# Kernel tuning notes

Measured on AMD Instinct MI355X. Metric: run time of the kernel, lower is better.

The kernel has to match this reference:

```python
import jax, jax.numpy as jnp
import numpy as np

B = 1024      # num graphs
NPG = 128     # nodes per graph
N = B * NPG
EPG = 512     # edges per graph
E = B * EPG
D = 64
MAX_STEPS = 4
S = MAX_STEPS + 1   # max_steps + stop-step offset
T = 1.0
TB = 1.0
NEG = -1e30
STOP = -1


def setup_inputs() -> dict:
    key = jax.random.key(0)
    ks = jax.random.split(key, 24)
    edge_batch = jnp.repeat(jnp.arange(B, dtype=jnp.int32), EPG)
    src = jax.random.randint(ks[0], (E,), 0, NPG, dtype=jnp.int32) + edge_batch * NPG
    dst = jax.random.randint(ks[1], (E,), 0, NPG, dtype=jnp.int32) + edge_batch * NPG
    edge_index = jnp.stack([src, dst])
    sc = 1.0 / np.sqrt(D)
    p = lambda k, shape: (jax.random.normal(k, shape, jnp.float32) * sc)
    return dict(
        node_tokens=p(ks[2], (N, D)), edge_emb=p(ks[3], (E, D)),
        Wf1=p(ks[4], (D, D)), Wnf=p(ks[5], (D, D)), Wf2=p(ks[6], (D, D)),
        bf=jnp.zeros((D,), jnp.float32), wf=p(ks[7], (D,)),
        Wb1=p(ks[8], (D, D)), Wnb=p(ks[9], (D, D)), Wb2=p(ks[10], (D, D)),
        bb=jnp.zeros((D,), jnp.float32), wb=p(ks[11], (D,)),
        w_stop=p(ks[12], (D,)), b_stop=jnp.zeros((), jnp.float32),
        Ws=p(ks[13], (D, D)), Wu=p(ks[14], (D, D)), bu=jnp.zeros((D,), jnp.float32),
        edge_index=edge_index, edge_batch=edge_batch,
    )


def reference(node_tokens, edge_emb, Wf1, Wnf, Wf2, bf, wf,
              Wb1, Wnb, Wb2, bb, wb, w_stop, b_stop, Ws, Wu, bu,
              edge_index, edge_batch):
    esrc, edst = edge_index[0], edge_index[1]
    # state-independent part of the edge scores (precomputed once; faithful math)
    base_f = edge_emb @ Wf1 + node_tokens[esrc] @ Wnf + bf   # [E,D]
    base_b = edge_emb @ Wb1 + node_tokens[edst] @ Wnb + bb   # [E,D]
    g_ids = jnp.arange(B, dtype=jnp.int32)
    eidx = jnp.arange(E, dtype=jnp.int32)

    def seg_lse(x, valid):
        # per-graph logsumexp over valid edges (grad-safe masking)
        xm = jnp.where(valid, x, NEG)
        m = jax.ops.segment_max(xm, edge_batch, num_segments=B)
        xc = jnp.where(valid, x - m[edge_batch], 0.0)
        s = jax.ops.segment_sum(jnp.where(valid, jnp.exp(xc), 0.0), edge_batch, num_segments=B)
        return m + jnp.log(jnp.maximum(s, 1e-30))

    def step_fn(carry, k):
        state_vec, active, used, done, steps, stopn = carry
        valid = (esrc == active[edge_batch]) & (~used) & (~done[edge_batch])
        allow_stop = (~done) & (steps < MAX_STEPS)
        # forward edge scores + stop logit
        h = jax.nn.relu(base_f + (state_vec @ Wf2)[edge_batch])   # [E,D]
        score = h @ wf                                            # [E]
        stop_logit = state_vec @ w_stop + b_stop                  # [B]
        x = score / T
        lse_e = seg_lse(x, valid)
        stop_t = jnp.where(allow_stop, stop_logit / T, NEG)
        Z = jnp.logaddexp(lse_e, stop_t)
        logp_edge = x - Z[edge_batch]
        logp_stop = jnp.where(allow_stop, stop_logit / T - Z, 0.0)
        has_edge = jax.ops.segment_sum(valid.astype(jnp.int32), edge_batch, num_segments=B) > 0
        # gumbel-max sampling with scatter_max semantics
        ke, ksn = jax.random.split(k)
        se = jnp.where(valid, logp_edge + jax.random.gumbel(ke, (E,)), NEG)
        ss = jnp.where(allow_stop, logp_stop + jax.random.gumbel(ksn, (B,)), NEG)
        m = jax.ops.segment_max(se, edge_batch, num_segments=B)
        amax = jax.ops.segment_min(jnp.where(se == m[edge_batch], eidx, E), edge_batch, num_segments=B)
        amax = jnp.where(has_edge, amax, 0).astype(jnp.int32)
        m = jnp.where(has_edge, m, NEG)
        choose_stop = (ss > m) | (~has_edge)
        actions = jnp.where(choose_stop | done, STOP, amax)
        log_pf = jnp.where(choose_stop, logp_stop, logp_edge[amax])
        log_pf = jnp.where(done, 0.0, log_pf)
        take_edge = (actions >= 0) & (~done)
        stopping = choose_stop & (~done)
        stopn = jnp.where((stopn < 0) & stopping, active - g_ids * NPG, stopn)
        # state encoder update (masked)
        rel = edge_emb[amax]                                      # [B,D]
        new_state = jnp.tanh(state_vec @ Ws + rel @ Wu + bu)
        state_vec = jnp.where(take_edge[:, None], new_state, state_vec)
        # env step
        new_active = jnp.where(take_edge, edst[amax], active)
        used = used.at[amax].max(take_edge)
        steps = steps + take_edge.astype(jnp.int32)
        new_done = done | stopping
        # backward policy log-prob over edges incoming to the new active node
        bvalid = edst == new_active[edge_batch]
        hb = jax.nn.relu(base_b + (state_vec @ Wb2)[edge_batch])
        xb = (hb @ wb) / TB
        lse_b = seg_lse(xb, bvalid)
        log_pb = jnp.where(take_edge, xb[amax] - lse_b, 0.0)
        return (state_vec, new_active, used, new_done, steps, stopn), (actions, log_pf, log_pb)

    init = (
        jnp.zeros((B, D), jnp.float32),      # state_vec
        g_ids * NPG,                          # active node (global) = graph start node
        jnp.zeros((E,), bool),                # used_edge_mask
        jnp.zeros((B,), bool),                # done
        jnp.zeros((B,), jnp.int32),           # step_counts
        jnp.full((B,), STOP, jnp.int32),      # stop_node_locals
    )
    keys = jax.random.split(jax.random.key(42), S)
    (state_vec, active, used, done, steps, stopn), ys = jax.lax.scan(step_fn, init, keys)
    actions_seq = ys[0].T      # [B,S]
    log_pf_steps = ys[1].T     # [B,S]
    log_pb_steps = ys[2].T     # [B,S]
    stopn = jnp.where(stopn < 0, active - g_ids * NPG, stopn)   # backfill stop nodes
    return (actions_seq, log_pf_steps.sum(1), log_pf_steps, log_pb_steps,
            used, stopn, steps.astype(jnp.float32))
```

## Files before the change

### kernel.cpp

```cpp
#include <hip/hip_runtime.h>
#include <hip/hip_bf16.h>
#include <cstdint>

#define NBLK 1024
#define NPG  128
#define EPG  512
#define DD   64
#define NSTEP 5
#define ETOT (NBLK*EPG)
#define NEGF (-1e30f)
#define WAVES 4
#define MAXDEG 32

#define OA  0
#define OLS 5120
#define OPF 6144
#define OPB 11264
#define OU  16384
#define OSN 540672
#define OST 541696

struct KeysArg {
  uint32_t ke0[NSTEP], ke1[NSTEP];
  uint32_t ks0[NSTEP], ks1[NSTEP];
};

__host__ __device__ inline uint32_t rotl32(uint32_t x, int r){ return (x<<r)|(x>>(32-r)); }

__host__ __device__ inline void tf2x32(uint32_t k0, uint32_t k1, uint32_t& x0, uint32_t& x1){
  uint32_t k2 = k0 ^ k1 ^ 0x1BD11BDAu;
  x0 += k0; x1 += k1;
  x0+=x1; x1=rotl32(x1,13); x1^=x0;
  x0+=x1; x1=rotl32(x1,15); x1^=x0;
  x0+=x1; x1=rotl32(x1,26); x1^=x0;
  x0+=x1; x1=rotl32(x1, 6); x1^=x0;
  x0+=k1; x1+=k2+1u;
  x0+=x1; x1=rotl32(x1,17); x1^=x0;
  x0+=x1; x1=rotl32(x1,29); x1^=x0;
  x0+=x1; x1=rotl32(x1,16); x1^=x0;
  x0+=x1; x1=rotl32(x1,24); x1^=x0;
  x0+=k2; x1+=k0+2u;
  x0+=x1; x1=rotl32(x1,13); x1^=x0;
  x0+=x1; x1=rotl32(x1,15); x1^=x0;
  x0+=x1; x1=rotl32(x1,26); x1^=x0;
  x0+=x1; x1=rotl32(x1, 6); x1^=x0;
  x0+=k0; x1+=k1+3u;
  x0+=x1; x1=rotl32(x1,17); x1^=x0;
  x0+=x1; x1=rotl32(x1,29); x1^=x0;
  x0+=x1; x1=rotl32(x1,16); x1^=x0;
  x0+=x1; x1=rotl32(x1,24); x1^=x0;
  x0+=k1; x1+=k2+4u;
  x0+=x1; x1=rotl32(x1,13); x1^=x0;
  x0+=x1; x1=rotl32(x1,15); x1^=x0;
  x0+=x1; x1=rotl32(x1,26); x1^=x0;
  x0+=x1; x1=rotl32(x1, 6); x1^=x0;
  x0+=k2; x1+=k0+5u;
}

__device__ inline float gumbel_from_bits(uint32_t bits){
  float f = __uint_as_float((bits>>9) | 0x3f800000u) - 1.0f;
  const float tiny = 1.17549435e-38f;
  float u = fmaxf(tiny, f * (1.0f - tiny) + tiny);
  return -logf(-logf(u));
}

__device__ inline float gumbel_part(uint32_t k0, uint32_t k1, uint32_t idx){
  uint32_t x0 = 0u, x1 = idx;
  tf2x32(k0, k1, x0, x1);
  return gumbel_from_bits(x0 ^ x1);
}

__device__ inline float wsum(float x){
  #pragma unroll
  for (int off = 32; off; off >>= 1) x += __shfl_xor(x, off, 64);
  return x;
}

__device__ __forceinline__ void wsum4(float& x0, float& x1, float& x2, float& x3){
  #pragma unroll
  for (int off = 32; off; off >>= 1){
    x0 += __shfl_xor(x0, off, 64);
    x1 += __shfl_xor(x1, off, 64);
    x2 += __shfl_xor(x2, off, 64);
    x3 += __shfl_xor(x3, off, 64);
  }
}

__device__ __forceinline__ float rdlane(float v, int i){
  return __int_as_float(__builtin_amdgcn_readlane(__float_as_int(v), i));
}
__device__ __forceinline__ int rdlane_i(int v, int i){
  return __builtin_amdgcn_readlane(v, i);
}

__device__ __forceinline__ float matvec_col(const float* __restrict__ W, float v, int lane){
  float a0=0.f, a1=0.f, a2=0.f, a3=0.f;
  #pragma unroll 8
  for (int i = 0; i < DD; i += 4){
    a0 = fmaf(rdlane(v, i  ), W[(i  )*DD+lane], a0);
    a1 = fmaf(rdlane(v, i+1), W[(i+1)*DD+lane], a1);
    a2 = fmaf(rdlane(v, i+2), W[(i+2)*DD+lane], a2);
    a3 = fmaf(rdlane(v, i+3), W[(i+3)*DD+lane], a3);
  }
  return (a0+a1)+(a2+a3);
}

__device__ __forceinline__ void matvec4(const float* __restrict__ W,
                                        float v0, float v1, float v2, float v3,
                                        int lane, float o[4]){
  float acc[4][4] = {{0,0,0,0},{0,0,0,0},{0,0,0,0},{0,0,0,0}};
  #pragma unroll 8
  for (int i = 0; i < DD; i += 4){
    #pragma unroll
    for (int t = 0; t < 4; t++){
      float w  = W[(i+t)*DD+lane];
      acc[0][t] = fmaf(rdlane(v0, i+t), w, acc[0][t]);
      acc[1][t] = fmaf(rdlane(v1, i+t), w, acc[1][t]);
      acc[2][t] = fmaf(rdlane(v2, i+t), w, acc[2][t]);
      acc[3][t] = fmaf(rdlane(v3, i+t), w, acc[3][t]);
    }
  }
  #pragma unroll
  for (int c = 0; c < 4; c++)
    o[c] = (acc[c][0]+acc[c][1])+(acc[c][2]+acc[c][3]);
}

__global__ void __launch_bounds__(256, 4)
gfn_fused(const float* __restrict__ node_tokens,
          const float* __restrict__ edge_emb,
          const float* __restrict__ Wf1, const float* __restrict__ Wnf, const float* __restrict__ Wf2,
          const float* __restrict__ bf,  const float* __restrict__ wf,
          const float* __restrict__ Wb1, const float* __restrict__ Wnb, const float* __restrict__ Wb2,
          const float* __restrict__ bb,  const float* __restrict__ wb,
          const float* __restrict__ w_stop, const float* __restrict__ b_stop,
          const float* __restrict__ Ws,  const float* __restrict__ Wu, const float* __restrict__ bu,
          const int* __restrict__ e_src, const int* __restrict__ e_dst,
          float* __restrict__ out, KeysArg keys)
{
  const int g    = blockIdx.x;
  const int tid  = threadIdx.x;
  const int lane = tid & 63;
  const int wave = tid >> 6;
  const int ebase = g * EPG;

  __shared__ uint8_t  srcL[EPG], dstL[EPG];
  __shared__ uint16_t listO[EPG], listI[EPG];
  __shared__ int cntO[NPG], cntI[NPG], begO[NPG], begI[NPG];
  __shared__ uint8_t usedL[EPG];
  __shared__ float st_sh[DD];
  __shared__ float u_sh[DD], nt_sh[DD], acs_sh[DD];
  __shared__ float ntb_sh[DD], ntN_sh[DD], uN_sh[DD], ubB_sh[DD];
  __shared__ float xcF[MAXDEG], gmF[MAXDEG], xcB[MAXDEG];
  __shared__ float sl_sh, xbb_sh;

  for (int j = tid; j < EPG; j += 256){
    srcL[j] = (uint8_t)(e_src[ebase+j] - g*NPG);
    dstL[j] = (uint8_t)(e_dst[ebase+j] - g*NPG);
    usedL[j] = 0;
  }
  for (int n = tid; n < NPG; n += 256){ cntO[n]=0; cntI[n]=0; }
  if (tid < DD) st_sh[tid] = 0.f;
  __syncthreads();

  for (int j = tid; j < EPG; j += 256){
    atomicAdd(&cntO[srcL[j]], 1);
    atomicAdd(&cntI[dstL[j]], 1);
  }
  __syncthreads();

  if (wave == 0){
    int n0 = lane*2, n1 = n0+1;
    int c0O=cntO[n0], c1O=cntO[n1], sO=c0O+c1O;
    int c0I=cntI[n0], c1I=cntI[n1], sI=c0I+c1I;
    int xO=sO, xI=sI;
    #pragma unroll
    for (int off=1; off<64; off<<=1){
      int tO=__shfl_up(xO,off,64), tI=__shfl_up(xI,off,64);
      if (lane>=off){ xO+=tO; xI+=tI; }
    }
    begO[n0]=xO-sO; begO[n1]=xO-c1O;
    begI[n0]=xI-sI; begI[n1]=xI-c1I;
  }
  __syncthreads();
  for (int n = tid; n < NPG; n += 256){ cntO[n]=0; cntI[n]=0; }
  __syncthreads();

  for (int ph = 0; ph < WAVES; ph++){
    if (wave == ph){
      #pragma unroll
      for (int h = 0; h < 2; h++){
        int j = ph*128 + h*64 + lane;
        int sL = srcL[j]; int p = atomicAdd(&cntO[sL],1); listO[begO[sL]+p] = (uint16_t)j;
        int dL = dstL[j]; int q = atomicAdd(&cntI[dL],1); listI[begI[dL]+q] = (uint16_t)j;
      }
    }
    __syncthreads();
  }

  const float bf_l = bf[lane], wf_l = wf[lane];
  const float bb_l = bb[lane], wb_l = wb[lane];
  const float bu_l = bu[lane], wst_l = w_stop[lane];
  const float bstop = b_stop[0];

  float gsv;
  {
    uint32_t k0 = keys.ks0[0], k1 = keys.ks1[0];
    #pragma unroll
    for (int s5 = 1; s5 < NSTEP; s5++)
      if (lane == s5){ k0 = keys.ks0[s5]; k1 = keys.ks1[s5]; }
    gsv = (lane < NSTEP) ? gumbel_part(k0, k1, (uint32_t)g) : 0.f;
  }

  bool done = false;
  int stepsC = 0, stopn = -1, activeL = 0;
  float lpf_sum = 0.f;
  int bOF = begO[0], dOF = min(cntO[0], MAXDEG);

  {
    float st_v = st_sh[lane];
    if (wave == 0)      u_sh[lane]   = matvec_col(Wf2, st_v, lane);
    else if (wave == 1){ float ntv = node_tokens[(size_t)(g*NPG+0)*DD+lane];
                         nt_sh[lane] = matvec_col(Wnf, ntv, lane); }
    else if (wave == 2) acs_sh[lane] = matvec_col(Ws, st_v, lane);
    else {
      float sl = wsum(st_v * wst_l) + bstop;
      if (lane == 0) sl_sh = sl;
      if (lane < dOF)
        gmF[lane] = gumbel_part(keys.ke0[0], keys.ke1[0], (uint32_t)(ebase + listO[bOF+lane]));
    }
    __syncthreads();
    if (wave >= 2){
      for (int c = wave-2; c < (dOF+3)>>2; c += 2){
        int el[4]; float v[4];
        #pragma unroll
        for (int t = 0; t < 4; t++){
          int k = c*4 + t;
          el[t] = listO[bOF + min(k, dOF-1)];
          v[t]  = edge_emb[(size_t)(ebase+el[t])*DD + lane];
        }
        float o[4], x[4];
        matvec4(Wf1, v[0], v[1], v[2], v[3], lane, o);
        #pragma unroll
        for (int t = 0; t < 4; t++) x[t] = fmaxf(o[t] + nt_sh[lane] + bf_l + u_sh[lane], 0.f) * wf_l;
        wsum4(x[0], x[1], x[2], x[3]);
        #pragma unroll
        for (int t = 0; t < 4; t++){
          int k = c*4 + t;
          if (k < dOF && lane == 0) xcF[k] = usedL[el[t]] ? NEGF : x[t];
        }
      }
    }
    __syncthreads();
  }

  for (int s = 0; s < NSTEP; s++){
    float act_out = -1.f, lpf_out = 0.f, lpb_out = 0.f;
    if (!done){
      float xr = (lane < MAXDEG) ? xcF[lane] : NEGF;
      float gr = (lane < MAXDEG) ? gmF[lane] : 0.f;
      int   er = (lane < dOF)    ? (int)listO[bOF + lane] : -1;
      float sl = sl_sh;

      float m1 = NEGF; int nvalid = 0;
      for (int k=0;k<dOF;k++){ float xk=rdlane(xr,k); if (xk!=NEGF){ m1=fmaxf(m1,xk); nvalid++; } }
      float ex = expf(xr - m1);
      float ssum = 0.f;
      for (int k=0;k<dOF;k++){ float xk=rdlane(xr,k); if (xk!=NEGF) ssum += rdlane(ex,k); }
      const bool has_edge = nvalid > 0;
      float lse_e = m1 + logf(fmaxf(ssum, 1e-30f));
      const bool allow_stop = (stepsC < 4);
      float stop_t = allow_stop ? sl : NEGF;
      float amx = fmaxf(lse_e, stop_t);
      float Z = amx + log1pf(expf(-fabsf(lse_e - stop_t)));

      float mbest = NEGF; int elbest = -1; float xbest = 0.f;
      for (int k=0;k<dOF;k++){
        float xk = rdlane(xr,k);
        if (xk == NEGF) continue;
        float se = (xk - Z) + rdlane(gr,k);
        if (se > mbest){ mbest = se; elbest = rdlane_i(er,k); xbest = xk; }
      }
      float gs = rdlane(gsv, s);
      float ss = allow_stop ? (sl - Z) + gs : NEGF;
      float mcmp = has_edge ? mbest : NEGF;
      const bool choose_stop = (ss > mcmp) || (!has_edge);
      float logp_stop = allow_stop ? (sl - Z) : 0.f;
      const bool take_edge = !choose_stop;

      act_out = choose_stop ? -1.f : (float)(ebase + elbest);
      lpf_out = choose_stop ? logp_stop : (xbest - Z);
      if (choose_stop && stopn < 0) stopn = activeL;

      if (take_edge){
        const int newA = dstL[elbest];
        const bool more = (s < NSTEP-1);
        const int bI  = begI[newA], dIc = min(cntI[newA], MAXDEG);
        const int bON = begO[newA];
        const int dON = more ? min(cntO[newA], MAXDEG) : 0;

        float vPre[4]; int elPre[4]; bool pre = false; int c0;
        if (wave == 2 || wave == 0){
          c0 = (wave==2 ? 0 : 1);
          if (c0 < ((dIc+3)>>2)){
            pre = true;
            #pragma unroll
            for (int t = 0; t < 4; t++){
              int k = c0*4 + t;
              elPre[t] = listI[bI + min(k, dIc-1)];
              vPre[t]  = edge_emb[(size_t)(ebase+elPre[t])*DD + lane];
            }
          }
        } else {
          c0 = (wave==3 ? 0 : 1);
          if (c0 < ((dON+3)>>2)){
            pre = true;
            #pragma unroll
            for (int t = 0; t < 4; t++){
              int k = c0*4 + t;
              elPre[t] = listO[bON + min(k, dON-1)];
              vPre[t]  = edge_emb[(size_t)(ebase+elPre[t])*DD + lane];
            }
          }
        }

        if (wave == 0){
          float rv = edge_emb[(size_t)(ebase+elbest)*DD + lane];
          float acr = matvec_col(Wu, rv, lane);
          st_sh[lane] = tanhf(acs_sh[lane] + acr + bu_l);
          if (lane == 0) usedL[elbest] = 1;
        } else if (wave == 1){
          float nbv = node_tokens[(size_t)(g*NPG + newA)*DD + lane];
          ntb_sh[lane] = matvec_col(Wnb, nbv, lane);
        } else if (wave == 2){
          if (more){
            float nbv = node_tokens[(size_t)(g*NPG + newA)*DD + lane];
            ntN_sh[lane] = matvec_col(Wnf, nbv, lane);
          }
        }
        activeL = newA; stepsC++;
        __syncthreads();

        float stp = st_sh[lane];
        if (wave == 0){
          if (more) uN_sh[lane] = matvec_col(Wf2, stp, lane);
        } else if (wave == 1){
          ubB_sh[lane] = matvec_col(Wb2, stp, lane);
        } else if (wave == 2){
          if (more) acs_sh[lane] = matvec_col(Ws, stp, lane);
        } else {
          if (more){
            float s2 = wsum(stp * wst_l) + bstop;
            if (lane == 0) sl_sh = s2;
            if (lane < dON)
              gmF[lane] = gumbel_part(keys.ke0[s+1], keys.ke1[s+1],
                                      (uint32_t)(ebase + listO[bON+lane]));
          }
        }
        __syncthreads();

        if (wave == 2 || wave == 0){
          for (int c = c0; c < (dIc+3)>>2; c += 2){
            int el[4]; float v[4];
            if (pre && c == c0){
              #pragma unroll
              for (int t = 0; t < 4; t++){ el[t] = elPre[t]; v[t] = vPre[t]; }
            } else {
              #pragma unroll
              for (int t = 0; t < 4; t++){
                int k = c*4 + t;
                el[t] = listI[bI + min(k, dIc-1)];
                v[t]  = edge_emb[(size_t)(ebase+el[t])*DD + lane];
              }
            }
            float o[4], xb[4];
            matvec4(Wb1, v[0], v[1], v[2], v[3], lane, o);
            #pragma unroll
            for (int t = 0; t < 4; t++) xb[t] = fmaxf(o[t] + ntb_sh[lane] + bb_l + ubB_sh[lane], 0.f) * wb_l;
            wsum4(xb[0], xb[1], xb[2], xb[3]);
            #pragma unroll
            for (int t = 0; t < 4; t++){
              int k = c*4 + t;
              if (k < dIc && lane == 0){
                xcB[k] = xb[t];
                if (el[t] == elbest) xbb_sh = xb[t];
              }
            }
          }
        } else {
          for (int c = c0; c < (dON+3)>>2; c += 2){
            int el[4]; float v[4];
            if (pre && c == c0){
              #pragma unroll
              for (int t = 0; t < 4; t++){ el[t] = elPre[t]; v[t] = vPre[t]; }
            } else {
              #pragma unroll
              for (int t = 0; t < 4; t++){
                int k = c*4 + t;
                el[t] = listO[bON + min(k, dON-1)];
                v[t]  = edge_emb[(size_t)(ebase+el[t])*DD + lane];
              }
            }
            float o[4], x[4];
            matvec4(Wf1, v[0], v[1], v[2], v[3], lane, o);
            #pragma unroll
            for (int t = 0; t < 4; t++) x[t] = fmaxf(o[t] + ntN_sh[lane] + bf_l + uN_sh[lane], 0.f) * wf_l;
            wsum4(x[0], x[1], x[2], x[3]);
            #pragma unroll
            for (int t = 0; t < 4; t++){
              int k = c*4 + t;
              if (k < dON && lane == 0) xcF[k] = usedL[el[t]] ? NEGF : x[t];
            }
          }
        }
        __syncthreads();

        float xbr = (lane < MAXDEG) ? xcB[lane] : 0.f;
        float m2 = NEGF;
        for (int k=0;k<dIc;k++) m2 = fmaxf(m2, rdlane(xbr,k));
        float ex2 = expf(xbr - m2);
        float s2 = 0.f;
        for (int k=0;k<dIc;k++) s2 += rdlane(ex2,k);
        float lse_b = m2 + logf(fmaxf(s2, 1e-30f));
        lpb_out = xbb_sh - lse_b;

        bOF = bON; dOF = dON;
      }
      done = done || choose_stop;
    }

    if (tid == 0){
      out[OA  + g*NSTEP + s] = act_out;
      out[OPF + g*NSTEP + s] = lpf_out;
      out[OPB + g*NSTEP + s] = lpb_out;
    }
    lpf_sum += lpf_out;
  }

  if (tid == 0){
    out[OLS + g] = lpf_sum;
    int sn = (stopn < 0) ? activeL : stopn;
    out[OSN + g] = (float)sn;
    out[OST + g] = (float)stepsC;
  }
  for (int j = tid; j < EPG; j += 256)
    out[OU + ebase + j] = usedL[j] ? 1.0f : 0.0f;
}

extern "C" void kernel_launch(void* const* d_in, const int* in_sizes, int n_in,
                              void* d_out, int out_size, void* d_ws, size_t ws_size,
                              hipStream_t stream)
{
  (void)in_sizes; (void)n_in; (void)out_size; (void)d_ws; (void)ws_size;

  KeysArg K;
  for (uint32_t s = 0; s < NSTEP; s++){
    uint32_t a = 0u, b = s;
    tf2x32(0u, 42u, a, b);
    uint32_t e0 = 0u, e1 = 0u;
    tf2x32(a, b, e0, e1);
    uint32_t s0 = 0u, s1 = 1u;
    tf2x32(a, b, s0, s1);
    K.ke0[s] = e0; K.ke1[s] = e1;
    K.ks0[s] = s0; K.ks1[s] = s1;
  }

  const int* eidx = (const int*)d_in[17];
  gfn_fused<<<dim3(NBLK), dim3(256), 0, stream>>>(
      (const float*)d_in[0],  (const float*)d_in[1],
      (const float*)d_in[2],  (const float*)d_in[3],  (const float*)d_in[4],
      (const float*)d_in[5],  (const float*)d_in[6],
      (const float*)d_in[7],  (const float*)d_in[8],  (const float*)d_in[9],
      (const float*)d_in[10], (const float*)d_in[11],
      (const float*)d_in[12], (const float*)d_in[13],
      (const float*)d_in[14], (const float*)d_in[15], (const float*)d_in[16],
      eidx, eidx + ETOT,
      (float*)d_out, K);
}
```

Measured before the change: 78.35 us.

## Replicate per-step state matvecs in every wave and cut barriers to one per step

Each wave now computes the state update, stop logit, gumbel noise and its own node/state projections redundantly in registers, so the shared-memory staging buffers go away. The score buffers are double-buffered by step parity, which lets each step run with a single __syncthreads instead of three. The forward masking now also excludes the just-chosen edge locally, because usedL may not be visible yet. The cost is more redundant matvec work per wave, which raises ALU load and register pressure in exchange for fewer barrier stalls.

```diff
diff --git a/kernel.cpp b/kernel.cpp
--- a/kernel.cpp
+++ b/kernel.cpp
@@ -142,16 +142,15 @@
   const int lane = tid & 63;
   const int wave = tid >> 6;
   const int ebase = g * EPG;
+  const bool isBwd = (wave == 0) || (wave == 2);
 
   __shared__ uint8_t  srcL[EPG], dstL[EPG];
   __shared__ uint16_t listO[EPG], listI[EPG];
   __shared__ int cntO[NPG], cntI[NPG], begO[NPG], begI[NPG];
   __shared__ uint8_t usedL[EPG];
-  __shared__ float st_sh[DD];
-  __shared__ float u_sh[DD], nt_sh[DD], acs_sh[DD];
-  __shared__ float ntb_sh[DD], ntN_sh[DD], uN_sh[DD], ubB_sh[DD];
-  __shared__ float xcF[MAXDEG], gmF[MAXDEG], xcB[MAXDEG];
-  __shared__ float sl_sh, xbb_sh;
+  __shared__ float xcF[2][MAXDEG];
+  __shared__ float xcB[2][MAXDEG];
+  __shared__ float xbb_sh[2];
 
   for (int j = tid; j < EPG; j += 256){
     srcL[j] = (uint8_t)(e_src[ebase+j] - g*NPG);
@@ -159,7 +158,6 @@
     usedL[j] = 0;
   }
   for (int n = tid; n < NPG; n += 256){ cntO[n]=0; cntI[n]=0; }
-  if (tid < DD) st_sh[tid] = 0.f;
   __syncthreads();
 
   for (int j = tid; j < EPG; j += 256){
@@ -216,21 +214,20 @@
   float lpf_sum = 0.f;
   int bOF = begO[0], dOF = min(cntO[0], MAXDEG);
 
+  float st_v = 0.f;
+  float acs_reg, sl_reg, gm_reg;
+
   {
-    float st_v = st_sh[lane];
-    if (wave == 0)      u_sh[lane]   = matvec_col(Wf2, st_v, lane);
-    else if (wave == 1){ float ntv = node_tokens[(size_t)(g*NPG+0)*DD+lane];
-                         nt_sh[lane] = matvec_col(Wnf, ntv, lane); }
-    else if (wave == 2) acs_sh[lane] = matvec_col(Ws, st_v, lane);
-    else {
-      float sl = wsum(st_v * wst_l) + bstop;
-      if (lane == 0) sl_sh = sl;
-      if (lane < dOF)
-        gmF[lane] = gumbel_part(keys.ke0[0], keys.ke1[0], (uint32_t)(ebase + listO[bOF+lane]));
-    }
-    __syncthreads();
-    if (wave >= 2){
-      for (int c = wave-2; c < (dOF+3)>>2; c += 2){
+    float u0  = matvec_col(Wf2, st_v, lane);
+    float ntv = node_tokens[(size_t)(g*NPG + 0)*DD + lane];
+    float nt0 = matvec_col(Wnf, ntv, lane);
+    acs_reg = matvec_col(Ws, st_v, lane);
+    sl_reg  = wsum(st_v * wst_l) + bstop;
+    gm_reg  = (lane < dOF)
+            ? gumbel_part(keys.ke0[0], keys.ke1[0], (uint32_t)(ebase + listO[bOF+lane]))
+            : 0.f;
+    if (!isBwd){
+      for (int c = (wave==3 ? 0 : 1); c < (dOF+3)>>2; c += 2){
         int el[4]; float v[4];
         #pragma unroll
         for (int t = 0; t < 4; t++){
@@ -241,12 +238,12 @@
         float o[4], x[4];
         matvec4(Wf1, v[0], v[1], v[2], v[3], lane, o);
         #pragma unroll
-        for (int t = 0; t < 4; t++) x[t] = fmaxf(o[t] + nt_sh[lane] + bf_l + u_sh[lane], 0.f) * wf_l;
+        for (int t = 0; t < 4; t++) x[t] = fmaxf(o[t] + nt0 + bf_l + u0, 0.f) * wf_l;
         wsum4(x[0], x[1], x[2], x[3]);
         #pragma unroll
         for (int t = 0; t < 4; t++){
           int k = c*4 + t;
-          if (k < dOF && lane == 0) xcF[k] = usedL[el[t]] ? NEGF : x[t];
+          if (k < dOF && lane == 0) xcF[0][k] = usedL[el[t]] ? NEGF : x[t];
         }
       }
     }
@@ -254,12 +251,15 @@
   }
 
   for (int s = 0; s < NSTEP; s++){
+    const int par = s & 1;
     float act_out = -1.f, lpf_out = 0.f, lpb_out = 0.f;
+    bool take_edge = false, stopped_now = false;
+    int dIc = 0;
+
     if (!done){
-      float xr = (lane < MAXDEG) ? xcF[lane] : NEGF;
-      float gr = (lane < MAXDEG) ? gmF[lane] : 0.f;
+      float xr = (lane < MAXDEG) ? xcF[par][lane] : NEGF;
       int   er = (lane < dOF)    ? (int)listO[bOF + lane] : -1;
-      float sl = sl_sh;
+      float sl = sl_reg;
 
       float m1 = NEGF; int nvalid = 0;
       for (int k=0;k<dOF;k++){ float xk=rdlane(xr,k); if (xk!=NEGF){ m1=fmaxf(m1,xk); nvalid++; } }
@@ -277,7 +277,7 @@
       for (int k=0;k<dOF;k++){
         float xk = rdlane(xr,k);
         if (xk == NEGF) continue;
-        float se = (xk - Z) + rdlane(gr,k);
+        float se = (xk - Z) + rdlane(gm_reg,k);
         if (se > mbest){ mbest = se; elbest = rdlane_i(er,k); xbest = xk; }
       }
       float gs = rdlane(gsv, s);
@@ -285,7 +285,8 @@
       float mcmp = has_edge ? mbest : NEGF;
       const bool choose_stop = (ss > mcmp) || (!has_edge);
       float logp_stop = allow_stop ? (sl - Z) : 0.f;
-      const bool take_edge = !choose_stop;
+      take_edge = !choose_stop;
+      stopped_now = choose_stop;
 
       act_out = choose_stop ? -1.f : (float)(ebase + elbest);
       lpf_out = choose_stop ? logp_stop : (xbest - Z);
@@ -294,13 +295,15 @@
       if (take_edge){
         const int newA = dstL[elbest];
         const bool more = (s < NSTEP-1);
-        const int bI  = begI[newA], dIc = min(cntI[newA], MAXDEG);
+        const int bI  = begI[newA]; dIc = min(cntI[newA], MAXDEG);
         const int bON = begO[newA];
         const int dON = more ? min(cntO[newA], MAXDEG) : 0;
 
-        float vPre[4]; int elPre[4]; bool pre = false; int c0;
-        if (wave == 2 || wave == 0){
-          c0 = (wave==2 ? 0 : 1);
+        float rv  = edge_emb[(size_t)(ebase+elbest)*DD + lane];
+        float nbv = node_tokens[(size_t)(g*NPG + newA)*DD + lane];
+        float vPre[4]; int elPre[4]; bool pre = false; int c0 = 0;
+        if (isBwd){
+          c0 = (wave==0 ? 0 : 1);
           if (c0 < ((dIc+3)>>2)){
             pre = true;
             #pragma unroll
@@ -310,7 +313,7 @@
               vPre[t]  = edge_emb[(size_t)(ebase+elPre[t])*DD + lane];
             }
           }
-        } else {
+        } else if (more){
           c0 = (wave==3 ? 0 : 1);
           if (c0 < ((dON+3)>>2)){
             pre = true;
@@ -323,42 +326,28 @@
           }
         }
 
-        if (wave == 0){
-          float rv = edge_emb[(size_t)(ebase+elbest)*DD + lane];
-          float acr = matvec_col(Wu, rv, lane);
-          st_sh[lane] = tanhf(acs_sh[lane] + acr + bu_l);
-          if (lane == 0) usedL[elbest] = 1;
-        } else if (wave == 1){
-          float nbv = node_tokens[(size_t)(g*NPG + newA)*DD + lane];
-          ntb_sh[lane] = matvec_col(Wnb, nbv, lane);
-        } else if (wave == 2){
-          if (more){
-            float nbv = node_tokens[(size_t)(g*NPG + newA)*DD + lane];
-            ntN_sh[lane] = matvec_col(Wnf, nbv, lane);
-          }
-        }
+        float acr = matvec_col(Wu, rv, lane);
+        st_v = tanhf(acs_reg + acr + bu_l);
+        float d1 = 0.f, d2 = 0.f;
+        if (isBwd){
+          d1 = matvec_col(Wnb, nbv, lane);
+          d2 = matvec_col(Wb2, st_v, lane);
+        } else if (more){
+          d1 = matvec_col(Wnf, nbv, lane);
+          d2 = matvec_col(Wf2, st_v, lane);
+        }
+        if (more){
+          acs_reg = matvec_col(Ws, st_v, lane);
+          sl_reg  = wsum(st_v * wst_l) + bstop;
+          gm_reg  = (lane < dON)
+                  ? gumbel_part(keys.ke0[s+1], keys.ke1[s+1],
+                                (uint32_t)(ebase + listO[bON+lane]))
+                  : 0.f;
+        }
+        if (tid == 0) usedL[elbest] = 1;
         activeL = newA; stepsC++;
-        __syncthreads();
-
-        float stp = st_sh[lane];
-        if (wave == 0){
-          if (more) uN_sh[lane] = matvec_col(Wf2, stp, lane);
-        } else if (wave == 1){
-          ubB_sh[lane] = matvec_col(Wb2, stp, lane);
-        } else if (wave == 2){
-          if (more) acs_sh[lane] = matvec_col(Ws, stp, lane);
-        } else {
-          if (more){
-            float s2 = wsum(stp * wst_l) + bstop;
-            if (lane == 0) sl_sh = s2;
-            if (lane < dON)
-              gmF[lane] = gumbel_part(keys.ke0[s+1], keys.ke1[s+1],
-                                      (uint32_t)(ebase + listO[bON+lane]));
-          }
-        }
-        __syncthreads();
-
-        if (wave == 2 || wave == 0){
+
+        if (isBwd){
           for (int c = c0; c < (dIc+3)>>2; c += 2){
             int el[4]; float v[4];
             if (pre && c == c0){
@@ -375,18 +364,18 @@
             float o[4], xb[4];
             matvec4(Wb1, v[0], v[1], v[2], v[3], lane, o);
             #pragma unroll
-            for (int t = 0; t < 4; t++) xb[t] = fmaxf(o[t] + ntb_sh[lane] + bb_l + ubB_sh[lane], 0.f) * wb_l;
+            for (int t = 0; t < 4; t++) xb[t] = fmaxf(o[t] + d1 + bb_l + d2, 0.f) * wb_l;
             wsum4(xb[0], xb[1], xb[2], xb[3]);
             #pragma unroll
             for (int t = 0; t < 4; t++){
               int k = c*4 + t;
               if (k < dIc && lane == 0){
-                xcB[k] = xb[t];
-                if (el[t] == elbest) xbb_sh = xb[t];
+                xcB[par][k] = xb[t];
+                if (el[t] == elbest) xbb_sh[par] = xb[t];
               }
             }
           }
-        } else {
+        } else if (more){
           for (int c = c0; c < (dON+3)>>2; c += 2){
             int el[4]; float v[4];
             if (pre && c == c0){
@@ -403,30 +392,33 @@
             float o[4], x[4];
             matvec4(Wf1, v[0], v[1], v[2], v[3], lane, o);
             #pragma unroll
-            for (int t = 0; t < 4; t++) x[t] = fmaxf(o[t] + ntN_sh[lane] + bf_l + uN_sh[lane], 0.f) * wf_l;
+            for (int t = 0; t < 4; t++) x[t] = fmaxf(o[t] + d1 + bf_l + d2, 0.f) * wf_l;
             wsum4(x[0], x[1], x[2], x[3]);
             #pragma unroll
             for (int t = 0; t < 4; t++){
               int k = c*4 + t;
-              if (k < dON && lane == 0) xcF[k] = usedL[el[t]] ? NEGF : x[t];
+              if (k < dON && lane == 0)
+                xcF[par^1][k] = (usedL[el[t]] || el[t] == elbest) ? NEGF : x[t];
             }
           }
         }
-        __syncthreads();
-
-        float xbr = (lane < MAXDEG) ? xcB[lane] : 0.f;
-        float m2 = NEGF;
-        for (int k=0;k<dIc;k++) m2 = fmaxf(m2, rdlane(xbr,k));
-        float ex2 = expf(xbr - m2);
-        float s2 = 0.f;
-        for (int k=0;k<dIc;k++) s2 += rdlane(ex2,k);
-        float lse_b = m2 + logf(fmaxf(s2, 1e-30f));
-        lpb_out = xbb_sh - lse_b;
-
         bOF = bON; dOF = dON;
       }
-      done = done || choose_stop;
-    }
+    }
+
+    __syncthreads();
+
+    if (!done && take_edge){
+      float xbr = (lane < MAXDEG) ? xcB[par][lane] : 0.f;
+      float m2 = NEGF;
+      for (int k=0;k<dIc;k++) m2 = fmaxf(m2, rdlane(xbr,k));
+      float ex2 = expf(xbr - m2);
+      float s2 = 0.f;
+      for (int k=0;k<dIc;k++) s2 += rdlane(ex2,k);
+      float lse_b = m2 + logf(fmaxf(s2, 1e-30f));
+      lpb_out = xbb_sh[par] - lse_b;
+    }
+    done = done || stopped_now;
 
     if (tid == 0){
       out[OA  + g*NSTEP + s] = act_out;
```

Measured after the change: 96.08 us. 1.23x slower.

## Widen block to 8 waves and speculatively precompute per-candidate-edge matvecs

Applied to the files above, without the earlier changes.

Doubles the block to 512 threads and dedicates extra waves to precompute, for every candidate outgoing edge, the Wu, Wnb and Wnf matvecs of the edge embedding and destination node token, stored in shared memory. Once the edge is chosen, the state update and node projections become lookups rather than serial matvecs on the critical path. Part of the backward and forward edge-score matvecs is also started before the barrier to overlap with the state matvecs. In exchange it does extra speculative work for edges that are never chosen, uses more shared memory and registers, and launches with a 512-thread occupancy hint of 6 blocks.

```diff
diff --git a/kernel.cpp b/kernel.cpp
--- a/kernel.cpp
+++ b/kernel.cpp
@@ -9,8 +9,8 @@
 #define NSTEP 5
 #define ETOT (NBLK*EPG)
 #define NEGF (-1e30f)
-#define WAVES 4
 #define MAXDEG 32
+#define TPB 512
 
 #define OA  0
 #define OLS 5120
@@ -125,7 +125,7 @@
     o[c] = (acc[c][0]+acc[c][1])+(acc[c][2]+acc[c][3]);
 }
 
-__global__ void __launch_bounds__(256, 4)
+__global__ void __launch_bounds__(512, 6)
 gfn_fused(const float* __restrict__ node_tokens,
           const float* __restrict__ edge_emb,
           const float* __restrict__ Wf1, const float* __restrict__ Wnf, const float* __restrict__ Wf2,
@@ -147,22 +147,22 @@
   __shared__ uint16_t listO[EPG], listI[EPG];
   __shared__ int cntO[NPG], cntI[NPG], begO[NPG], begI[NPG];
   __shared__ uint8_t usedL[EPG];
-  __shared__ float st_sh[DD];
-  __shared__ float u_sh[DD], nt_sh[DD], acs_sh[DD];
-  __shared__ float ntb_sh[DD], ntN_sh[DD], uN_sh[DD], ubB_sh[DD];
+  __shared__ float uN_sh[DD], ubB_sh[DD], acs_sh[DD], ntN_sh[DD];
+  __shared__ float wuv[MAXDEG][DD];
+  __shared__ float wnbv[MAXDEG][DD];
+  __shared__ float wnfv[MAXDEG][DD];
   __shared__ float xcF[MAXDEG], gmF[MAXDEG], xcB[MAXDEG];
   __shared__ float sl_sh, xbb_sh;
 
-  for (int j = tid; j < EPG; j += 256){
+  for (int j = tid; j < EPG; j += TPB){
     srcL[j] = (uint8_t)(e_src[ebase+j] - g*NPG);
     dstL[j] = (uint8_t)(e_dst[ebase+j] - g*NPG);
     usedL[j] = 0;
   }
-  for (int n = tid; n < NPG; n += 256){ cntO[n]=0; cntI[n]=0; }
-  if (tid < DD) st_sh[tid] = 0.f;
+  for (int n = tid; n < NPG; n += TPB){ cntO[n]=0; cntI[n]=0; }
   __syncthreads();
 
-  for (int j = tid; j < EPG; j += 256){
+  for (int j = tid; j < EPG; j += TPB){
     atomicAdd(&cntO[srcL[j]], 1);
     atomicAdd(&cntI[dstL[j]], 1);
   }
@@ -182,17 +182,14 @@
     begI[n0]=xI-sI; begI[n1]=xI-c1I;
   }
   __syncthreads();
-  for (int n = tid; n < NPG; n += 256){ cntO[n]=0; cntI[n]=0; }
+  for (int n = tid; n < NPG; n += TPB){ cntO[n]=0; cntI[n]=0; }
   __syncthreads();
 
-  for (int ph = 0; ph < WAVES; ph++){
+  for (int ph = 0; ph < 8; ph++){
     if (wave == ph){
-      #pragma unroll
-      for (int h = 0; h < 2; h++){
-        int j = ph*128 + h*64 + lane;
-        int sL = srcL[j]; int p = atomicAdd(&cntO[sL],1); listO[begO[sL]+p] = (uint16_t)j;
-        int dL = dstL[j]; int q = atomicAdd(&cntI[dL],1); listI[begI[dL]+q] = (uint16_t)j;
-      }
+      int j = ph*64 + lane;
+      int sL = srcL[j]; int p = atomicAdd(&cntO[sL],1); listO[begO[sL]+p] = (uint16_t)j;
+      int dL = dstL[j]; int q = atomicAdd(&cntI[dL],1); listI[begI[dL]+q] = (uint16_t)j;
     }
     __syncthreads();
   }
@@ -217,37 +214,69 @@
   int bOF = begO[0], dOF = min(cntO[0], MAXDEG);
 
   {
-    float st_v = st_sh[lane];
-    if (wave == 0)      u_sh[lane]   = matvec_col(Wf2, st_v, lane);
-    else if (wave == 1){ float ntv = node_tokens[(size_t)(g*NPG+0)*DD+lane];
-                         nt_sh[lane] = matvec_col(Wnf, ntv, lane); }
-    else if (wave == 2) acs_sh[lane] = matvec_col(Ws, st_v, lane);
-    else {
-      float sl = wsum(st_v * wst_l) + bstop;
+    if (wave == 0)      uN_sh[lane] = matvec_col(Wf2, 0.f, lane);
+    else if (wave == 1){ float ntv = node_tokens[(size_t)(g*NPG)*DD + lane];
+                         ntN_sh[lane] = matvec_col(Wnf, ntv, lane); }
+    else if (wave == 2) acs_sh[lane] = matvec_col(Ws, 0.f, lane);
+    else if (wave == 3){
+      float sl = wsum(0.f * wst_l) + bstop;
       if (lane == 0) sl_sh = sl;
       if (lane < dOF)
         gmF[lane] = gumbel_part(keys.ke0[0], keys.ke1[0], (uint32_t)(ebase + listO[bOF+lane]));
     }
     __syncthreads();
-    if (wave >= 2){
-      for (int c = wave-2; c < (dOF+3)>>2; c += 2){
+    const int nfc = (dOF+3)>>2;
+    if (wave == 4){
+      for (int c = 0; c < nfc; c++){
         int el[4]; float v[4];
         #pragma unroll
         for (int t = 0; t < 4; t++){
-          int k = c*4 + t;
-          el[t] = listO[bOF + min(k, dOF-1)];
+          el[t] = listO[bOF + min(c*4+t, dOF-1)];
           v[t]  = edge_emb[(size_t)(ebase+el[t])*DD + lane];
         }
         float o[4], x[4];
         matvec4(Wf1, v[0], v[1], v[2], v[3], lane, o);
         #pragma unroll
-        for (int t = 0; t < 4; t++) x[t] = fmaxf(o[t] + nt_sh[lane] + bf_l + u_sh[lane], 0.f) * wf_l;
+        for (int t = 0; t < 4; t++) x[t] = fmaxf(o[t] + ntN_sh[lane] + bf_l + uN_sh[lane], 0.f) * wf_l;
         wsum4(x[0], x[1], x[2], x[3]);
         #pragma unroll
         for (int t = 0; t < 4; t++){
           int k = c*4 + t;
           if (k < dOF && lane == 0) xcF[k] = usedL[el[t]] ? NEGF : x[t];
         }
+      }
+    } else if (wave == 5){
+      for (int c = 0; c < nfc; c++){
+        float v[4];
+        #pragma unroll
+        for (int t = 0; t < 4; t++)
+          v[t] = edge_emb[(size_t)(ebase + listO[bOF + min(c*4+t, dOF-1)])*DD + lane];
+        float o[4];
+        matvec4(Wu, v[0], v[1], v[2], v[3], lane, o);
+        #pragma unroll
+        for (int t = 0; t < 4; t++){ int k = c*4+t; if (k < dOF) wuv[k][lane] = o[t]; }
+      }
+    } else if (wave == 6){
+      for (int c = 0; c < nfc; c++){
+        float v[4];
+        #pragma unroll
+        for (int t = 0; t < 4; t++)
+          v[t] = node_tokens[(size_t)(g*NPG + dstL[listO[bOF + min(c*4+t, dOF-1)]])*DD + lane];
+        float o[4];
+        matvec4(Wnb, v[0], v[1], v[2], v[3], lane, o);
+        #pragma unroll
+        for (int t = 0; t < 4; t++){ int k = c*4+t; if (k < dOF) wnbv[k][lane] = o[t]; }
+      }
+    } else if (wave == 7){
+      for (int c = 0; c < nfc; c++){
+        float v[4];
+        #pragma unroll
+        for (int t = 0; t < 4; t++)
+          v[t] = node_tokens[(size_t)(g*NPG + dstL[listO[bOF + min(c*4+t, dOF-1)]])*DD + lane];
+        float o[4];
+        matvec4(Wnf, v[0], v[1], v[2], v[3], lane, o);
+        #pragma unroll
+        for (int t = 0; t < 4; t++){ int k = c*4+t; if (k < dOF) wnfv[k][lane] = o[t]; }
       }
     }
     __syncthreads();
@@ -273,12 +302,12 @@
       float amx = fmaxf(lse_e, stop_t);
       float Z = amx + log1pf(expf(-fabsf(lse_e - stop_t)));
 
-      float mbest = NEGF; int elbest = -1; float xbest = 0.f;
+      float mbest = NEGF; int elbest = -1, kbest = -1; float xbest = 0.f;
       for (int k=0;k<dOF;k++){
         float xk = rdlane(xr,k);
         if (xk == NEGF) continue;
         float se = (xk - Z) + rdlane(gr,k);
-        if (se > mbest){ mbest = se; elbest = rdlane_i(er,k); xbest = xk; }
+        if (se > mbest){ mbest = se; elbest = rdlane_i(er,k); kbest = k; xbest = xk; }
       }
       float gs = rdlane(gsv, s);
       float ss = allow_stop ? (sl - Z) + gs : NEGF;
@@ -297,57 +326,31 @@
         const int bI  = begI[newA], dIc = min(cntI[newA], MAXDEG);
         const int bON = begO[newA];
         const int dON = more ? min(cntO[newA], MAXDEG) : 0;
-
-        float vPre[4]; int elPre[4]; bool pre = false; int c0;
-        if (wave == 2 || wave == 0){
-          c0 = (wave==2 ? 0 : 1);
-          if (c0 < ((dIc+3)>>2)){
-            pre = true;
-            #pragma unroll
-            for (int t = 0; t < 4; t++){
-              int k = c0*4 + t;
-              elPre[t] = listI[bI + min(k, dIc-1)];
-              vPre[t]  = edge_emb[(size_t)(ebase+elPre[t])*DD + lane];
-            }
-          }
-        } else {
-          c0 = (wave==3 ? 0 : 1);
-          if (c0 < ((dON+3)>>2)){
-            pre = true;
-            #pragma unroll
-            for (int t = 0; t < 4; t++){
-              int k = c0*4 + t;
-              elPre[t] = listO[bON + min(k, dON-1)];
-              vPre[t]  = edge_emb[(size_t)(ebase+elPre[t])*DD + lane];
-            }
-          }
-        }
-
-        if (wave == 0){
-          float rv = edge_emb[(size_t)(ebase+elbest)*DD + lane];
-          float acr = matvec_col(Wu, rv, lane);
-          st_sh[lane] = tanhf(acs_sh[lane] + acr + bu_l);
-          if (lane == 0) usedL[elbest] = 1;
-        } else if (wave == 1){
-          float nbv = node_tokens[(size_t)(g*NPG + newA)*DD + lane];
-          ntb_sh[lane] = matvec_col(Wnb, nbv, lane);
-        } else if (wave == 2){
-          if (more){
-            float nbv = node_tokens[(size_t)(g*NPG + newA)*DD + lane];
-            ntN_sh[lane] = matvec_col(Wnf, nbv, lane);
-          }
-        }
+        const int nbc = (dIc+3)>>2;
+        const int nfc = (dON+3)>>2;
+
+        float wnbv_k = wnbv[kbest][lane];
+        float wnfv_k = more ? wnfv[kbest][lane] : 0.f;
+        float stp = tanhf(acs_sh[lane] + wuv[kbest][lane] + bu_l);
         activeL = newA; stepsC++;
         __syncthreads();
 
-        float stp = st_sh[lane];
+        float oB0[4], oF0[4], oF1[4];
         if (wave == 0){
+          if (lane == 0) usedL[elbest] = 1;
           if (more) uN_sh[lane] = matvec_col(Wf2, stp, lane);
         } else if (wave == 1){
           ubB_sh[lane] = matvec_col(Wb2, stp, lane);
         } else if (wave == 2){
           if (more) acs_sh[lane] = matvec_col(Ws, stp, lane);
-        } else {
+          if (nbc > 1){
+            float v[4];
+            #pragma unroll
+            for (int t = 0; t < 4; t++)
+              v[t] = edge_emb[(size_t)(ebase + listI[bI + min(4+t, dIc-1)])*DD + lane];
+            matvec4(Wb1, v[0], v[1], v[2], v[3], lane, oB0);
+          }
+        } else if (wave == 3){
           if (more){
             float s2 = wsum(stp * wst_l) + bstop;
             if (lane == 0) sl_sh = s2;
@@ -355,60 +358,121 @@
               gmF[lane] = gumbel_part(keys.ke0[s+1], keys.ke1[s+1],
                                       (uint32_t)(ebase + listO[bON+lane]));
           }
+          {
+            float v[4];
+            #pragma unroll
+            for (int t = 0; t < 4; t++)
+              v[t] = edge_emb[(size_t)(ebase + listI[bI + min(t, dIc-1)])*DD + lane];
+            matvec4(Wb1, v[0], v[1], v[2], v[3], lane, oB0);
+          }
+        } else if (wave == 4 && more){
+          for (int c = 0; c < min(nfc,2); c++){
+            float v[4];
+            #pragma unroll
+            for (int t = 0; t < 4; t++)
+              v[t] = edge_emb[(size_t)(ebase + listO[bON + min(c*4+t, dON-1)])*DD + lane];
+            matvec4(Wf1, v[0], v[1], v[2], v[3], lane, (c==0)?oF0:oF1);
+          }
+        } else if (wave == 5 && more){
+          for (int c = 0; c < nfc; c++){
+            float v[4];
+            #pragma unroll
+            for (int t = 0; t < 4; t++)
+              v[t] = edge_emb[(size_t)(ebase + listO[bON + min(c*4+t, dON-1)])*DD + lane];
+            float o[4];
+            matvec4(Wu, v[0], v[1], v[2], v[3], lane, o);
+            #pragma unroll
+            for (int t = 0; t < 4; t++){ int k = c*4+t; if (k < dON) wuv[k][lane] = o[t]; }
+          }
+        } else if (wave == 6 && more){
+          for (int c = 0; c < nfc; c++){
+            float v[4];
+            #pragma unroll
+            for (int t = 0; t < 4; t++)
+              v[t] = node_tokens[(size_t)(g*NPG + dstL[listO[bON + min(c*4+t, dON-1)]])*DD + lane];
+            float o[4];
+            matvec4(Wnb, v[0], v[1], v[2], v[3], lane, o);
+            #pragma unroll
+            for (int t = 0; t < 4; t++){ int k = c*4+t; if (k < dON) wnbv[k][lane] = o[t]; }
+          }
+        } else if (wave == 7 && more){
+          for (int c = 0; c < nfc; c++){
+            float v[4];
+            #pragma unroll
+            for (int t = 0; t < 4; t++)
+              v[t] = node_tokens[(size_t)(g*NPG + dstL[listO[bON + min(c*4+t, dON-1)]])*DD + lane];
+            float o[4];
+            matvec4(Wnf, v[0], v[1], v[2], v[3], lane, o);
+            #pragma unroll
+            for (int t = 0; t < 4; t++){ int k = c*4+t; if (k < dON) wnfv[k][lane] = o[t]; }
+          }
         }
         __syncthreads();
 
-        if (wave == 2 || wave == 0){
-          for (int c = c0; c < (dIc+3)>>2; c += 2){
-            int el[4]; float v[4];
-            if (pre && c == c0){
-              #pragma unroll
-              for (int t = 0; t < 4; t++){ el[t] = elPre[t]; v[t] = vPre[t]; }
-            } else {
-              #pragma unroll
-              for (int t = 0; t < 4; t++){
-                int k = c*4 + t;
-                el[t] = listI[bI + min(k, dIc-1)];
-                v[t]  = edge_emb[(size_t)(ebase+el[t])*DD + lane];
+        if (wave == 2 || wave == 3){
+          const int myc = (wave == 3) ? 0 : 1;
+          if (myc < nbc){
+            float xb[4];
+            #pragma unroll
+            for (int t = 0; t < 4; t++) xb[t] = fmaxf(oB0[t] + wnbv_k + bb_l + ubB_sh[lane], 0.f) * wb_l;
+            wsum4(xb[0], xb[1], xb[2], xb[3]);
+            #pragma unroll
+            for (int t = 0; t < 4; t++){
+              int k = myc*4 + t;
+              if (k < dIc && lane == 0){
+                int el = listI[bI + k];
+                xcB[k] = xb[t];
+                if (el == elbest) xbb_sh = xb[t];
               }
             }
+          }
+          for (int c = 2 + ((wave==3)?0:1); c < nbc; c += 2){
+            float v[4];
+            #pragma unroll
+            for (int t = 0; t < 4; t++)
+              v[t] = edge_emb[(size_t)(ebase + listI[bI + min(c*4+t, dIc-1)])*DD + lane];
             float o[4], xb[4];
             matvec4(Wb1, v[0], v[1], v[2], v[3], lane, o);
             #pragma unroll
-            for (int t = 0; t < 4; t++) xb[t] = fmaxf(o[t] + ntb_sh[lane] + bb_l + ubB_sh[lane], 0.f) * wb_l;
+            for (int t = 0; t < 4; t++) xb[t] = fmaxf(o[t] + wnbv_k + bb_l + ubB_sh[lane], 0.f) * wb_l;
             wsum4(xb[0], xb[1], xb[2], xb[3]);
             #pragma unroll
             for (int t = 0; t < 4; t++){
               int k = c*4 + t;
               if (k < dIc && lane == 0){
+                int el = listI[bI + k];
                 xcB[k] = xb[t];
-                if (el[t] == elbest) xbb_sh = xb[t];
+                if (el == elbest) xbb_sh = xb[t];
               }
             }
           }
-        } else {
-          for (int c = c0; c < (dON+3)>>2; c += 2){
-            int el[4]; float v[4];
-            if (pre && c == c0){
-              #pragma unroll
-              for (int t = 0; t < 4; t++){ el[t] = elPre[t]; v[t] = vPre[t]; }
-            } else {
-              #pragma unroll
-              for (int t = 0; t < 4; t++){
-                int k = c*4 + t;
-                el[t] = listO[bON + min(k, dON-1)];
-                v[t]  = edge_emb[(size_t)(ebase+el[t])*DD + lane];
-              }
+        } else if (wave == 4 && more){
+          for (int c = 0; c < min(nfc,2); c++){
+            float* o = (c==0) ? oF0 : oF1;
+            float x[4];
+            #pragma unroll
+            for (int t = 0; t < 4; t++) x[t] = fmaxf(o[t] + wnfv_k + bf_l + uN_sh[lane], 0.f) * wf_l;
+            wsum4(x[0], x[1], x[2], x[3]);
+            #pragma unroll
+            for (int t = 0; t < 4; t++){
+              int k = c*4 + t;
+              if (k < dON && lane == 0) xcF[k] = usedL[listO[bON + k]] ? NEGF : x[t];
             }
+          }
+          for (int c = 2; c < nfc; c++){
+            float v[4];
+            #pragma unroll
+            for (int t = 0; t < 4; t++)
+              v[t] = edge_emb[(size_t)(ebase + listO[bON + min(c*4+t, dON-1)])*DD + lane];
             float o[4], x[4];
             matvec4(Wf1, v[0], v[1], v[2], v[3], lane, o);
             #pragma unroll
-            for (int t = 0; t < 4; t++) x[t] = fmaxf(o[t] + ntN_sh[lane] + bf_l + uN_sh[lane], 0.f) * wf_l;
+            for (int t = 0; t < 4; t++) x[t] = fmaxf(o[t] + wnfv_k + bf_l + uN_sh[lane], 0.f) * wf_l;
             wsum4(x[0], x[1], x[2], x[3]);
             #pragma unroll
             for (int t = 0; t < 4; t++){
               int k = c*4 + t;
-              if (k < dON && lane == 0) xcF[k] = usedL[el[t]] ? NEGF : x[t];
+              if (k < dON && lane == 0) xcF[k] = usedL[listO[bON + k]] ? NEGF : x[t];
             }
           }
         }
@@ -442,7 +506,7 @@
     out[OSN + g] = (float)sn;
     out[OST + g] = (float)stepsC;
   }
-  for (int j = tid; j < EPG; j += 256)
+  for (int j = tid; j < EPG; j += TPB)
     out[OU + ebase + j] = usedL[j] ? 1.0f : 0.0f;
 }
 
@@ -465,7 +529,7 @@
   }
 
   const int* eidx = (const int*)d_in[17];
-  gfn_fused<<<dim3(NBLK), dim3(256), 0, stream>>>(
+  gfn_fused<<<dim3(NBLK), dim3(TPB), 0, stream>>>(
       (const float*)d_in[0],  (const float*)d_in[1],
       (const float*)d_in[2],  (const float*)d_in[3],  (const float*)d_in[4],
       (const float*)d_in[5],  (const float*)d_in[6],
```

New measurement: 124.1 us. +58.4%, slower.
